# Performance work log

Hardware: AMD Instinct MI355X
Metric: run time of the kernel (lower is better)

Reference implementation:

```python
import jax, jax.numpy as jnp
import numpy as np

B, S, E = 2, 2048, 1024
H = 16
D = E // H  # head_dim = 64
SCALE = D ** -0.5


def _rope_cos_sin(seq_len, dim, dtype=jnp.float32):
    inv_freq = 1.0 / (10000.0 ** (jnp.arange(0, dim, 2, dtype=jnp.float32) / dim))
    pos = jnp.arange(seq_len, dtype=jnp.float32)
    freqs = pos[:, None] * inv_freq[None, :]  # [S, D/2]
    return jnp.cos(freqs).astype(dtype), jnp.sin(freqs).astype(dtype)


def _apply_rope(x, cos, sin):
    # x: [B, H, S, D]; interleaved complex rotation on (even, odd) pairs
    x2 = x.reshape(*x.shape[:-1], D // 2, 2)
    xr, xi = x2[..., 0], x2[..., 1]
    c = cos[None, None, :, :]
    s = sin[None, None, :, :]
    out_r = xr * c - xi * s
    out_i = xr * s + xi * c
    return jnp.stack([out_r, out_i], axis=-1).reshape(x.shape)


def setup_inputs() -> dict:
    key = jax.random.key(0)
    k1, k2, k3, k4, k5 = jax.random.split(key, 5)
    query = jax.random.normal(k1, (B, S, E), dtype=jnp.float32)
    key_t = jax.random.normal(k2, (B, S, E), dtype=jnp.float32)
    value = jax.random.normal(k3, (B, S, E), dtype=jnp.float32)
    w_qkv = jax.random.normal(k4, (3 * E, E), dtype=jnp.float32) * 0.02
    w_out = jax.random.normal(k5, (E, E), dtype=jnp.float32) * 0.02
    return {"query": query, "key": key_t, "value": value,
            "w_qkv": w_qkv, "w_out": w_out}


def reference(query, key, value, w_qkv, w_out):
    # Fused QKV projection from query only (matches original module)
    qkv = jnp.einsum('bse,fe->bsf', query, w_qkv)  # [B, S, 3E]
    q, k, v = jnp.split(qkv, 3, axis=-1)
    to_heads = lambda t: t.reshape(B, S, H, D).transpose(0, 2, 1, 3)  # [B,H,S,D]
    q, k, v = to_heads(q), to_heads(k), to_heads(v)

    cos, sin = _rope_cos_sin(S, D, q.dtype)
    q = _apply_rope(q, cos, sin)
    k = _apply_rope(k, cos, sin)

    # Standard scaled dot-product attention (eval mode, no mask, no dropout)
    attn = jnp.einsum('bhsd,bhtd->bhst', q, k) * SCALE
    attn = jax.nn.softmax(attn.astype(jnp.float32), axis=-1).astype(q.dtype)
    ctx = jnp.einsum('bhst,bhtd->bhsd', attn, v)  # [B,H,S,D]

    out = ctx.transpose(0, 2, 1, 3).reshape(B, S, E)
    return jnp.einsum('bse,fe->bsf', out, w_out)
```

## Files before the change

### kernel.cpp

```cpp
#include <hip/hip_runtime.h>
#include <math.h>

typedef __attribute__((ext_vector_type(8))) __bf16 bf16x8;
typedef __attribute__((ext_vector_type(4))) __bf16 bf16x4;
typedef __attribute__((ext_vector_type(4))) float f32x4;

constexpr int kBATCH = 2;
constexpr int kS = 2048;
constexpr int kE = 1024;
constexpr int kH = 16;
constexpr int kD = 64;
constexpr float kScale = 0.125f;
constexpr float kQScale = 0.125f * 1.44269504088896340736f;

__device__ inline void gl2lds16(const void* g, void* l) {
    __builtin_amdgcn_global_load_lds((const __attribute__((address_space(1))) void*)g,
                                     (__attribute__((address_space(3))) void*)l, 16, 0, 0);
}

__global__ __launch_bounds__(256) void cvt2_kernel(const float* __restrict__ a, __bf16* __restrict__ oa, int na,
                                                   const float* __restrict__ b, __bf16* __restrict__ ob) {
    int idx = (blockIdx.x * 256 + threadIdx.x) * 4;
    const float* src;
    __bf16* dst;
    if (idx < na) { src = a + idx; dst = oa + idx; }
    else          { src = b + (idx - na); dst = ob + (idx - na); }
    float4 f = *(const float4*)src;
    bf16x4 r;
    r[0] = (__bf16)f.x; r[1] = (__bf16)f.y; r[2] = (__bf16)f.z; r[3] = (__bf16)f.w;
    *(bf16x4*)dst = r;
}

template <int TN, typename TC>
__global__ __launch_bounds__(256) void gemm_bt_kernel(const __bf16* __restrict__ A,
                                                      const __bf16* __restrict__ W,
                                                      TC* __restrict__ C,
                                                      int M, int N, int K) {
    constexpr int NI = TN / 32;
    __shared__ __bf16 As[128 * 64] __attribute__((aligned(16)));
    __shared__ __bf16 Bs[TN * 64] __attribute__((aligned(16)));

    const int tid  = threadIdx.x;
    const int lane = tid & 63;
    const int quad = lane >> 4;
    const int l16  = lane & 15;
    const int rx   = l16 & 7;
    const int wave = tid >> 6;
    const int wm   = (wave >> 1) * 64;
    const int wn   = (wave & 1) * (TN / 2);
    const int m0   = blockIdx.y * 128;
    const int n0   = blockIdx.x * TN;

    const int srow8  = lane >> 3;
    const int schunk = ((lane & 7) ^ srow8) * 8;

    f32x4 zero = {0.f, 0.f, 0.f, 0.f};
    f32x4 acc[4][NI];
#pragma unroll
    for (int i = 0; i < 4; ++i)
#pragma unroll
        for (int j = 0; j < NI; ++j) acc[i][j] = zero;

    for (int kt = 0; kt < K; kt += 64) {
        __syncthreads();
#pragma unroll
        for (int i = 0; i < 4; ++i) {
            int rbase = wave * 32 + i * 8;
            gl2lds16(A + (size_t)(m0 + rbase + srow8) * K + kt + schunk, &As[rbase * 64]);
        }
#pragma unroll
        for (int i = 0; i < NI; ++i) {
            int rbase = wave * (TN / 4) + i * 8;
            gl2lds16(W + (size_t)(n0 + rbase + srow8) * K + kt + schunk, &Bs[rbase * 64]);
        }
        __syncthreads();

#pragma unroll
        for (int kk = 0; kk < 2; ++kk) {
            bf16x8 af[4], bf[NI];
#pragma unroll
            for (int mi = 0; mi < 4; ++mi)
                af[mi] = *(const bf16x8*)(&As[(wm + mi * 16 + l16) * 64 + (((kk * 4 + quad) ^ rx)) * 8]);
#pragma unroll
            for (int ni = 0; ni < NI; ++ni)
                bf[ni] = *(const bf16x8*)(&Bs[(wn + ni * 16 + l16) * 64 + (((kk * 4 + quad) ^ rx)) * 8]);
#pragma unroll
            for (int mi = 0; mi < 4; ++mi)
#pragma unroll
                for (int ni = 0; ni < NI; ++ni)
                    acc[mi][ni] = __builtin_amdgcn_mfma_f32_16x16x32_bf16(af[mi], bf[ni], acc[mi][ni], 0, 0, 0);
        }
    }

#pragma unroll
    for (int mi = 0; mi < 4; ++mi)
#pragma unroll
        for (int ni = 0; ni < NI; ++ni)
#pragma unroll
            for (int r = 0; r < 4; ++r) {
                int row = m0 + wm + mi * 16 + quad * 4 + r;
                int col = n0 + wn + ni * 16 + l16;
                C[(size_t)row * N + col] = (TC)acc[mi][ni][r];
            }
}

__global__ __launch_bounds__(256) void rope_vtrans_kernel(const __bf16* __restrict__ qkv,
                                                          __bf16* __restrict__ qd,
                                                          __bf16* __restrict__ kd,
                                                          __bf16* __restrict__ vt) {
    __shared__ __bf16 tile[64 * 72] __attribute__((aligned(16)));

    if (blockIdx.x < 8192) {
        int tid = blockIdx.x * 256 + threadIdx.x;
        int i = tid & 31;
        int h = (tid >> 5) & (kH - 1);
        int s = (tid >> 9) & (kS - 1);
        int b = tid >> 20;

        size_t rowbase = (size_t)(b * kS + s) * (3 * kE);
        int coff = h * kD + 2 * i;

        float qr = (float)qkv[rowbase + coff];
        float qi = (float)qkv[rowbase + coff + 1];
        float kr = (float)qkv[rowbase + kE + coff];
        float ki = (float)qkv[rowbase + kE + coff + 1];

        float inv = expf(-(float)i * (9.210340371976184f / 32.0f));
        float ang = (float)s * inv;
        float cv = cosf(ang);
        float sv = sinf(ang);

        size_t qbase = ((size_t)(b * kH + h) * kS + s) * kD + 2 * i;
        qd[qbase]     = (__bf16)(kQScale * (qr * cv - qi * sv));
        qd[qbase + 1] = (__bf16)(kQScale * (qr * sv + qi * cv));
        kd[qbase]     = (__bf16)(kr * cv - ki * sv);
        kd[qbase + 1] = (__bf16)(kr * sv + ki * cv);
    } else {
        int flat = blockIdx.x - 8192;
        int s0 = (flat & 31) * 64;
        int bh = flat >> 5;
        int b = bh >> 4, h = bh & 15;
        int tid = threadIdx.x;

#pragma unroll
        for (int p = 0; p < 2; ++p) {
            int c = tid + p * 256;
            int r = c >> 3, jc = c & 7;
            *(bf16x8*)&tile[r * 72 + jc * 8] =
                *(const bf16x8*)(qkv + (size_t)(b * kS + s0 + r) * (3 * kE) + 2 * kE + h * kD + jc * 8);
        }
        __syncthreads();
#pragma unroll
        for (int p = 0; p < 2; ++p) {
            int c = tid + p * 256;
            int d = c >> 3, jt = c & 7;
            bf16x8 v;
#pragma unroll
            for (int u = 0; u < 8; ++u) {
                int src = (jt >> 2) * 32 + ((u >> 2) << 4) + ((jt & 3) << 2) + (u & 3);
                v[u] = tile[src * 72 + d];
            }
            *(bf16x8*)(vt + (size_t)(bh * kD + d) * kS + s0 + jt * 8) = v;
        }
    }
}

__global__ __launch_bounds__(256, 4) void attn_kernel(const __bf16* __restrict__ qd,
                                                      const __bf16* __restrict__ kd,
                                                      const __bf16* __restrict__ vt,
                                                      __bf16* __restrict__ ctx,
                                                      const float* __restrict__ wout,
                                                      __bf16* __restrict__ woutb) {
    __shared__ __bf16 Ks[2][64 * 64] __attribute__((aligned(16)));
    __shared__ __bf16 Vs[2][64 * 64] __attribute__((aligned(16)));

    const int lane = threadIdx.x & 63;
    const int wave = threadIdx.x >> 6;
    const int quad = lane >> 4;
    const int l16  = lane & 15;
    const int rx   = l16 & 7;

    {
        int base = blockIdx.x * 1024 + threadIdx.x * 4;
        float4 f = *(const float4*)(wout + base);
        bf16x4 r;
        r[0] = (__bf16)f.x; r[1] = (__bf16)f.y; r[2] = (__bf16)f.z; r[3] = (__bf16)f.w;
        *(bf16x4*)(woutb + base) = r;
    }

    const int flat = blockIdx.x;
    const int s    = flat >> 3;
    const int bh   = (flat & 7) * 4 + (s >> 5);
    const int q0   = (s & 31) * 64;
    const int b  = bh >> 4;
    const int h  = bh & 15;

    const __bf16* qp = qd + (size_t)bh * kS * kD;
    const __bf16* kp = kd + (size_t)bh * kS * kD;
    const __bf16* vp = vt + (size_t)bh * kD * kS;

    const int srow8  = lane >> 3;
    const int schunk = ((lane & 7) ^ srow8) * 8;

    bf16x8 aq0, aq1;
    {
        const __bf16* qrow = qp + (size_t)(q0 + wave * 16 + l16) * kD + quad * 8;
        aq0 = *(const bf16x8*)(qrow);
        aq1 = *(const bf16x8*)(qrow + 32);
    }

    bf16x8 vone;
#pragma unroll
    for (int u = 0; u < 8; ++u) vone[u] = (__bf16)1.0f;

    f32x4 zero = {0.f, 0.f, 0.f, 0.f};
    f32x4 acc[4];
    f32x4 asum = zero;
#pragma unroll
    for (int i = 0; i < 4; ++i) acc[i] = zero;

    int koff[4][2], voff[4][2];
#pragma unroll
    for (int g = 0; g < 4; ++g) {
        int row = g * 16 + l16;
        koff[g][0] = row * 64 + ((quad       ^ rx)) * 8;
        koff[g][1] = row * 64 + (((quad + 4) ^ rx)) * 8;
        voff[g][0] = row * 64 + ((quad       ^ (row & 7))) * 8;
        voff[g][1] = row * 64 + (((quad + 4) ^ (row & 7))) * 8;
    }

    const __bf16* kst[2];
    const __bf16* vst[2];
#pragma unroll
    for (int c = 0; c < 2; ++c) {
        int i = wave * 2 + c;
        kst[c] = kp + (size_t)(i * 8 + srow8) * kD + schunk;
        vst[c] = vp + (size_t)(i * 8 + srow8) * kS + schunk;
    }

#pragma unroll
    for (int c = 0; c < 2; ++c) {
        gl2lds16(kst[c], &Ks[0][(wave * 2 + c) * 512]);
        gl2lds16(vst[c], &Vs[0][(wave * 2 + c) * 512]);
        kst[c] += 64 * kD;
        vst[c] += 64;
    }

    const int nT = kS / 64;

    auto body = [&](int buf, bool prefetch) __attribute__((always_inline)) -> void {
        __syncthreads();
        if (prefetch) {
#pragma unroll
            for (int c = 0; c < 2; ++c) {
                gl2lds16(kst[c], &Ks[buf ^ 1][(wave * 2 + c) * 512]);
                gl2lds16(vst[c], &Vs[buf ^ 1][(wave * 2 + c) * 512]);
                kst[c] += 64 * kD;
                vst[c] += 64;
            }
        }

        f32x4 sg[4];
        __builtin_amdgcn_s_setprio(1);
#pragma unroll
        for (int g = 0; g < 4; ++g) {
            bf16x8 a0 = *(const bf16x8*)&Ks[buf][koff[g][0]];
            bf16x8 a1 = *(const bf16x8*)&Ks[buf][koff[g][1]];
            f32x4 t = __builtin_amdgcn_mfma_f32_16x16x32_bf16(a0, aq0, zero, 0, 0, 0);
            sg[g] = __builtin_amdgcn_mfma_f32_16x16x32_bf16(a1, aq1, t, 0, 0, 0);
        }
        __builtin_amdgcn_s_setprio(0);

        bf16x8 ap0, ap1;
#pragma unroll
        for (int r = 0; r < 4; ++r) {
            ap0[r]     = (__bf16)__builtin_amdgcn_exp2f(sg[0][r]);
            ap0[4 + r] = (__bf16)__builtin_amdgcn_exp2f(sg[1][r]);
            ap1[r]     = (__bf16)__builtin_amdgcn_exp2f(sg[2][r]);
            ap1[4 + r] = (__bf16)__builtin_amdgcn_exp2f(sg[3][r]);
        }

        __builtin_amdgcn_s_setprio(1);
        asum = __builtin_amdgcn_mfma_f32_16x16x32_bf16(ap0, vone, asum, 0, 0, 0);
        asum = __builtin_amdgcn_mfma_f32_16x16x32_bf16(ap1, vone, asum, 0, 0, 0);

#pragma unroll
        for (int nt = 0; nt < 4; ++nt) {
            bf16x8 bv0 = *(const bf16x8*)&Vs[buf][voff[nt][0]];
            bf16x8 bv1 = *(const bf16x8*)&Vs[buf][voff[nt][1]];
            acc[nt] = __builtin_amdgcn_mfma_f32_16x16x32_bf16(ap0, bv0, acc[nt], 0, 0, 0);
            acc[nt] = __builtin_amdgcn_mfma_f32_16x16x32_bf16(ap1, bv1, acc[nt], 0, 0, 0);
        }
        __builtin_amdgcn_s_setprio(0);
    };

    for (int it = 0; it < nT; it += 2) {
        body(0, true);
        body(1, it + 2 < nT);
    }

#pragma unroll
    for (int r = 0; r < 4; ++r) {
        float inv_l = 1.0f / asum[r];
        int srow_q = q0 + wave * 16 + quad * 4 + r;
#pragma unroll
        for (int nt = 0; nt < 4; ++nt) {
            int col = h * kD + nt * 16 + l16;
            ctx[(size_t)(b * kS + srow_q) * kE + col] = (__bf16)(acc[nt][r] * inv_l);
        }
    }
}

extern "C" void kernel_launch(void* const* d_in, const int* in_sizes, int n_in,
                              void* d_out, int out_size, void* d_ws, size_t ws_size,
                              hipStream_t stream) {
    const float* query = (const float*)d_in[0];
    const float* w_qkv = (const float*)d_in[3];
    const float* w_out = (const float*)d_in[4];
    float* out = (float*)d_out;

    const int M = kBATCH * kS;
    const int nQ = M * kE;
    const int nWqkv = 3 * kE * kE;

    char* ws = (char*)d_ws;
    __bf16* qkv_raw = (__bf16*)ws;
    __bf16* ctx     = (__bf16*)ws;
    __bf16* w_out_b = (__bf16*)(ws + (size_t)8388608);
    __bf16* qd      = (__bf16*)(ws + (size_t)25165824);
    __bf16* kd      = (__bf16*)(ws + (size_t)33554432);
    __bf16* vt      = (__bf16*)(ws + (size_t)41943040);
    __bf16* query_b = qd;
    __bf16* w_qkv_b = kd;

    cvt2_kernel<<<(nQ + nWqkv) / 1024, 256, 0, stream>>>(query, query_b, nQ, w_qkv, w_qkv_b);

    gemm_bt_kernel<128, __bf16>
        <<<dim3(3 * kE / 128, M / 128), 256, 0, stream>>>(query_b, w_qkv_b, qkv_raw, M, 3 * kE, kE);

    rope_vtrans_kernel<<<8192 + 1024, 256, 0, stream>>>(qkv_raw, qd, kd, vt);

    attn_kernel<<<1024, 256, 0, stream>>>(qd, kd, vt, ctx, w_out, w_out_b);

    gemm_bt_kernel<64, float>
        <<<dim3(kE / 64, M / 128), 256, 0, stream>>>(ctx, w_out_b, out, M, kE, kE);
}
```

Before: 203.6 us.

## Process 128 query rows per attention block to reuse K/V tiles

Each attention block now handles 128 query rows instead of 64, with every wave computing two 16-row query groups against the same K and V LDS tiles. The grid is halved to 512 blocks and the fused w_out conversion is rescaled to cover twice as many elements per block. This halves K/V global-to-LDS traffic and LDS reads per query row. In exchange, register pressure roughly doubles, which the lower launch-bound occupancy target (2 instead of 4) accounts for, and there are fewer blocks to spread across CUs.

```diff
diff --git a/kernel.cpp b/kernel.cpp
--- a/kernel.cpp
+++ b/kernel.cpp
@@ -165,7 +165,7 @@
     }
 }
 
-__global__ __launch_bounds__(256, 4) void attn_kernel(const __bf16* __restrict__ qd,
+__global__ __launch_bounds__(256, 2) void attn_kernel(const __bf16* __restrict__ qd,
                                                       const __bf16* __restrict__ kd,
                                                       const __bf16* __restrict__ vt,
                                                       __bf16* __restrict__ ctx,
@@ -181,17 +181,20 @@
     const int rx   = l16 & 7;
 
     {
-        int base = blockIdx.x * 1024 + threadIdx.x * 4;
-        float4 f = *(const float4*)(wout + base);
-        bf16x4 r;
-        r[0] = (__bf16)f.x; r[1] = (__bf16)f.y; r[2] = (__bf16)f.z; r[3] = (__bf16)f.w;
-        *(bf16x4*)(woutb + base) = r;
+        int base = blockIdx.x * 2048 + threadIdx.x * 8;
+#pragma unroll
+        for (int p = 0; p < 2; ++p) {
+            float4 f = *(const float4*)(wout + base + p * 4);
+            bf16x4 r;
+            r[0] = (__bf16)f.x; r[1] = (__bf16)f.y; r[2] = (__bf16)f.z; r[3] = (__bf16)f.w;
+            *(bf16x4*)(woutb + base + p * 4) = r;
+        }
     }
 
     const int flat = blockIdx.x;
     const int s    = flat >> 3;
-    const int bh   = (flat & 7) * 4 + (s >> 5);
-    const int q0   = (s & 31) * 64;
+    const int bh   = (flat & 7) * 4 + (s >> 4);
+    const int q0   = (s & 15) * 128;
     const int b  = bh >> 4;
     const int h  = bh & 15;
 
@@ -202,11 +205,12 @@
     const int srow8  = lane >> 3;
     const int schunk = ((lane & 7) ^ srow8) * 8;
 
-    bf16x8 aq0, aq1;
-    {
-        const __bf16* qrow = qp + (size_t)(q0 + wave * 16 + l16) * kD + quad * 8;
-        aq0 = *(const bf16x8*)(qrow);
-        aq1 = *(const bf16x8*)(qrow + 32);
+    bf16x8 aq[2][2];
+#pragma unroll
+    for (int qg = 0; qg < 2; ++qg) {
+        const __bf16* qrow = qp + (size_t)(q0 + wave * 32 + qg * 16 + l16) * kD + quad * 8;
+        aq[qg][0] = *(const bf16x8*)(qrow);
+        aq[qg][1] = *(const bf16x8*)(qrow + 32);
     }
 
     bf16x8 vone;
@@ -214,10 +218,12 @@
     for (int u = 0; u < 8; ++u) vone[u] = (__bf16)1.0f;
 
     f32x4 zero = {0.f, 0.f, 0.f, 0.f};
-    f32x4 acc[4];
-    f32x4 asum = zero;
-#pragma unroll
-    for (int i = 0; i < 4; ++i) acc[i] = zero;
+    f32x4 acc[2][4];
+    f32x4 asum[2] = {zero, zero};
+#pragma unroll
+    for (int qg = 0; qg < 2; ++qg)
+#pragma unroll
+        for (int i = 0; i < 4; ++i) acc[qg][i] = zero;
 
     int koff[4][2], voff[4][2];
 #pragma unroll
@@ -260,36 +266,47 @@
             }
         }
 
-        f32x4 sg[4];
+        f32x4 sg[2][4];
         __builtin_amdgcn_s_setprio(1);
 #pragma unroll
         for (int g = 0; g < 4; ++g) {
             bf16x8 a0 = *(const bf16x8*)&Ks[buf][koff[g][0]];
             bf16x8 a1 = *(const bf16x8*)&Ks[buf][koff[g][1]];
-            f32x4 t = __builtin_amdgcn_mfma_f32_16x16x32_bf16(a0, aq0, zero, 0, 0, 0);
-            sg[g] = __builtin_amdgcn_mfma_f32_16x16x32_bf16(a1, aq1, t, 0, 0, 0);
+#pragma unroll
+            for (int qg = 0; qg < 2; ++qg) {
+                f32x4 t = __builtin_amdgcn_mfma_f32_16x16x32_bf16(a0, aq[qg][0], zero, 0, 0, 0);
+                sg[qg][g] = __builtin_amdgcn_mfma_f32_16x16x32_bf16(a1, aq[qg][1], t, 0, 0, 0);
+            }
         }
         __builtin_amdgcn_s_setprio(0);
 
-        bf16x8 ap0, ap1;
-#pragma unroll
-        for (int r = 0; r < 4; ++r) {
-            ap0[r]     = (__bf16)__builtin_amdgcn_exp2f(sg[0][r]);
-            ap0[4 + r] = (__bf16)__builtin_amdgcn_exp2f(sg[1][r]);
-            ap1[r]     = (__bf16)__builtin_amdgcn_exp2f(sg[2][r]);
-            ap1[4 + r] = (__bf16)__builtin_amdgcn_exp2f(sg[3][r]);
-        }
+        bf16x8 ap[2][2];
+#pragma unroll
+        for (int qg = 0; qg < 2; ++qg)
+#pragma unroll
+            for (int r = 0; r < 4; ++r) {
+                ap[qg][0][r]     = (__bf16)__builtin_amdgcn_exp2f(sg[qg][0][r]);
+                ap[qg][0][4 + r] = (__bf16)__builtin_amdgcn_exp2f(sg[qg][1][r]);
+                ap[qg][1][r]     = (__bf16)__builtin_amdgcn_exp2f(sg[qg][2][r]);
+                ap[qg][1][4 + r] = (__bf16)__builtin_amdgcn_exp2f(sg[qg][3][r]);
+            }
 
         __builtin_amdgcn_s_setprio(1);
-        asum = __builtin_amdgcn_mfma_f32_16x16x32_bf16(ap0, vone, asum, 0, 0, 0);
-        asum = __builtin_amdgcn_mfma_f32_16x16x32_bf16(ap1, vone, asum, 0, 0, 0);
+#pragma unroll
+        for (int qg = 0; qg < 2; ++qg) {
+            asum[qg] = __builtin_amdgcn_mfma_f32_16x16x32_bf16(ap[qg][0], vone, asum[qg], 0, 0, 0);
+            asum[qg] = __builtin_amdgcn_mfma_f32_16x16x32_bf16(ap[qg][1], vone, asum[qg], 0, 0, 0);
+        }
 
 #pragma unroll
         for (int nt = 0; nt < 4; ++nt) {
             bf16x8 bv0 = *(const bf16x8*)&Vs[buf][voff[nt][0]];
             bf16x8 bv1 = *(const bf16x8*)&Vs[buf][voff[nt][1]];
-            acc[nt] = __builtin_amdgcn_mfma_f32_16x16x32_bf16(ap0, bv0, acc[nt], 0, 0, 0);
-            acc[nt] = __builtin_amdgcn_mfma_f32_16x16x32_bf16(ap1, bv1, acc[nt], 0, 0, 0);
+#pragma unroll
+            for (int qg = 0; qg < 2; ++qg) {
+                acc[qg][nt] = __builtin_amdgcn_mfma_f32_16x16x32_bf16(ap[qg][0], bv0, acc[qg][nt], 0, 0, 0);
+                acc[qg][nt] = __builtin_amdgcn_mfma_f32_16x16x32_bf16(ap[qg][1], bv1, acc[qg][nt], 0, 0, 0);
+            }
         }
         __builtin_amdgcn_s_setprio(0);
     };
@@ -300,15 +317,17 @@
     }
 
 #pragma unroll
-    for (int r = 0; r < 4; ++r) {
-        float inv_l = 1.0f / asum[r];
-        int srow_q = q0 + wave * 16 + quad * 4 + r;
-#pragma unroll
-        for (int nt = 0; nt < 4; ++nt) {
-            int col = h * kD + nt * 16 + l16;
-            ctx[(size_t)(b * kS + srow_q) * kE + col] = (__bf16)(acc[nt][r] * inv_l);
-        }
-    }
+    for (int qg = 0; qg < 2; ++qg)
+#pragma unroll
+        for (int r = 0; r < 4; ++r) {
+            float inv_l = 1.0f / asum[qg][r];
+            int srow_q = q0 + wave * 32 + qg * 16 + quad * 4 + r;
+#pragma unroll
+            for (int nt = 0; nt < 4; ++nt) {
+                int col = h * kD + nt * 16 + l16;
+                ctx[(size_t)(b * kS + srow_q) * kE + col] = (__bf16)(acc[qg][nt][r] * inv_l);
+            }
+        }
 }
 
 extern "C" void kernel_launch(void* const* d_in, const int* in_sizes, int n_in,
@@ -340,7 +359,7 @@
 
     rope_vtrans_kernel<<<8192 + 1024, 256, 0, stream>>>(qkv_raw, qd, kd, vt);
 
-    attn_kernel<<<1024, 256, 0, stream>>>(qd, kd, vt, ctx, w_out, w_out_b);
+    attn_kernel<<<512, 256, 0, stream>>>(qd, kd, vt, ctx, w_out, w_out_b);
 
     gemm_bt_kernel<64, float>
         <<<dim3(kE / 64, M / 128), 256, 0, stream>>>(ctx, w_out_b, out, M, kE, kE);
```

Measured after the change: 200.0 us. Within noise of the previous version (-1.8%).
